# Optimization experiments

Measured on AMD Instinct MI355X. Metric: run time of the kernel, lower is better.

Reference implementation:

```python
import jax, jax.numpy as jnp
import numpy as np

HID = 512
NB = 20
N = 65536
EPS = 1e-5


def layer_norm(x, g, b):
    m = jnp.mean(x, axis=-1, keepdims=True)
    v = jnp.mean(jnp.square(x - m), axis=-1, keepdims=True)
    return (x - m) * jax.lax.rsqrt(v + EPS) * g + b


def setup_inputs() -> dict:
    key = jax.random.key(0)
    ks = jax.random.split(key, 8)
    s = 0.02
    return {
        "x": jax.random.normal(ks[0], (N, 2), dtype=jnp.float32),
        "in_w": jax.random.normal(ks[1], (2, HID), dtype=jnp.float32) * s,
        "in_b": jnp.zeros((HID,), jnp.float32),
        "ln1_g": jnp.ones((NB, HID), jnp.float32),
        "ln1_b": jnp.zeros((NB, HID), jnp.float32),
        "fc1_w": jax.random.normal(ks[2], (NB, HID, HID), dtype=jnp.float32) * s,
        "fc1_b": jnp.zeros((NB, HID), jnp.float32),
        "ln2_g": jnp.ones((NB, HID), jnp.float32),
        "ln2_b": jnp.zeros((NB, HID), jnp.float32),
        "fc2_w": jax.random.normal(ks[3], (NB, HID, HID), dtype=jnp.float32) * s,
        "fc2_b": jnp.zeros((NB, HID), jnp.float32),
        "out_ln_g": jnp.ones((HID,), jnp.float32),
        "out_ln_b": jnp.zeros((HID,), jnp.float32),
        "out_w": jax.random.normal(ks[4], (HID, 1), dtype=jnp.float32) * s,
        "out_b": jnp.zeros((1,), jnp.float32),
    }


def reference(x, in_w, in_b, ln1_g, ln1_b, fc1_w, fc1_b, ln2_g, ln2_b,
              fc2_w, fc2_b, out_ln_g, out_ln_b, out_w, out_b):
    # in_proj + SiLU: [N,2] @ [2,HID]
    h = jax.nn.silu(x @ in_w + in_b)

    def block(h, p):
        g1, b1, w1, c1, g2, b2, w2, c2 = p
        t = jax.nn.silu(layer_norm(h, g1, b1) @ w1 + c1)
        t = layer_norm(t, g2, b2) @ w2 + c2
        return h + t, None

    h, _ = jax.lax.scan(block, h, (ln1_g, ln1_b, fc1_w, fc1_b,
                                   ln2_g, ln2_b, fc2_w, fc2_b))
    h = jax.nn.silu(layer_norm(h, out_ln_g, out_ln_b))
    return h @ out_w + out_b  # [N, 1]
```

## Files before the change

kernel.cpp:

```cpp
#include <hip/hip_runtime.h>


typedef float  fvec4 __attribute__((ext_vector_type(4)));
typedef __bf16 bvec8 __attribute__((ext_vector_type(8)));

#define HN_STRIDE 520
#define PL_STRIDE 67
#define N_PCOL    256
#define WCHUNK    16384
#define SMEM_BYTES (64*HN_STRIDE*2 + N_PCOL*PL_STRIDE*4 + 64*8)

__device__ __forceinline__ unsigned int f2bf(float v) {
    unsigned int u = __float_as_uint(v);
    return (u + 0x7fffu + ((u >> 16) & 1u)) >> 16;
}
__device__ __forceinline__ float silu_f(float v) {
    return v * (1.0f / (1.0f + __expf(-v)));
}

__global__ __launch_bounds__(256) void pack_weights(
        const float* __restrict__ w1, const float* __restrict__ w2,
        unsigned short* __restrict__ pk) {
    int tid = blockIdx.x * 256 + threadIdx.x;
    int l  = tid & 63;
    int f  = tid >> 6;
    int t  = f & 1;
    int kc = (f >> 1) & 15;
    int w  = (f >> 5) & 15;
    int g  = (f >> 9) & 1;
    int b  = f >> 10;
    const float* src = g ? w2 : w1;
    int k0 = kc * 32 + (l >> 4) * 8;
    int n  = w * 32 + (l & 15) * 2 + t;
    const float* s = src + ((size_t)b * 512 + k0) * 512 + n;
    unsigned int r[4];
#pragma unroll
    for (int j = 0; j < 4; ++j) {
        unsigned int lo = f2bf(s[(size_t)(2*j) * 512]);
        unsigned int hi = f2bf(s[(size_t)(2*j + 1) * 512]);
        r[j] = lo | (hi << 16);
    }
    *(uint4*)(pk + (size_t)tid * 8) = make_uint4(r[0], r[1], r[2], r[3]);
}

template <typename GetF>
__device__ __forceinline__ void ln_stats(GetF get, unsigned int* plane,
                                         float2* mv, int pcol, int q, int tid) {
#pragma unroll
    for (int rb = 0; rb < 4; ++rb)
#pragma unroll
        for (int i = 0; i < 4; ++i) {
            float v0 = get(rb, i, 0), v1 = get(rb, i, 1);
            float s  = v0 + v1;
            float ss = v0 * v0 + v1 * v1;
            int row = rb * 16 + q * 4 + i;
            plane[pcol * PL_STRIDE + row] = f2bf(s) | (f2bf(ss) << 16);
        }
    __syncthreads();
    if (tid < 512) {
        int r = tid >> 3, j = tid & 7;
        float s = 0.f, ss = 0.f;
#pragma unroll
        for (int u = 0; u < 32; ++u) {
            unsigned int pv = plane[(j + 8 * u) * PL_STRIDE + r];
            s  += __uint_as_float(pv << 16);
            ss += __uint_as_float(pv & 0xFFFF0000u);
        }
        s += __shfl_xor(s, 1); ss += __shfl_xor(ss, 1);
        s += __shfl_xor(s, 2); ss += __shfl_xor(ss, 2);
        s += __shfl_xor(s, 4); ss += __shfl_xor(ss, 4);
        if (j == 0) {
            float mean = s * (1.f / 512.f);
            float var  = ss * (1.f / 512.f) - mean * mean;
            mv[r] = make_float2(mean, rsqrtf(var + 1e-5f));
        }
    }
    __syncthreads();
}

template <typename GetF>
__device__ __forceinline__ void write_norm(GetF get, unsigned short* hn,
                                           const float2* mv, float2 g, float2 bv,
                                           int colbase, int q) {
#pragma unroll
    for (int rb = 0; rb < 4; ++rb)
#pragma unroll
        for (int i = 0; i < 4; ++i) {
            int row = rb * 16 + q * 4 + i;
            float2 m = mv[row];
            float v0 = (get(rb, i, 0) - m.x) * m.y * g.x + bv.x;
            float v1 = (get(rb, i, 1) - m.x) * m.y * g.y + bv.y;
            *(unsigned int*)(hn + row * HN_STRIDE + colbase) =
                f2bf(v0) | (f2bf(v1) << 16);
        }
    __syncthreads();
}

__device__ __forceinline__ void do_gemm(fvec4 acc[4][2],
                                        const unsigned short* hn,
                                        const unsigned short* __restrict__ wp,
                                        int l, int c, int q) {
#pragma unroll 2
    for (int kc = 0; kc < 16; ++kc) {
        bvec8 a[4], bb[2];
#pragma unroll
        for (int rb = 0; rb < 4; ++rb)
            a[rb] = *(const bvec8*)(hn + (rb * 16 + c) * HN_STRIDE + kc * 32 + q * 8);
#pragma unroll
        for (int t = 0; t < 2; ++t)
            bb[t] = *(const bvec8*)(wp + (kc * 2 + t) * 512 + l * 8);
#pragma unroll
        for (int rb = 0; rb < 4; ++rb)
#pragma unroll
            for (int t = 0; t < 2; ++t)
                acc[rb][t] = __builtin_amdgcn_mfma_f32_16x16x32_bf16(
                    a[rb], bb[t], acc[rb][t], 0, 0, 0);
    }
}

__global__ __launch_bounds__(1024, 4) void mlp_fused(
        const float* __restrict__ x,
        const float* __restrict__ in_w,  const float* __restrict__ in_b,
        const float* __restrict__ ln1_g, const float* __restrict__ ln1_b,
        const float* __restrict__ fc1_b,
        const float* __restrict__ ln2_g, const float* __restrict__ ln2_b,
        const float* __restrict__ fc2_b,
        const float* __restrict__ out_ln_g, const float* __restrict__ out_ln_b,
        const float* __restrict__ out_w, const float* __restrict__ out_b,
        const unsigned short* __restrict__ wpk,
        float* __restrict__ out) {
    extern __shared__ char smem[];
    unsigned short* hn = (unsigned short*)smem;
    unsigned int* plane = (unsigned int*)(smem + 64 * HN_STRIDE * 2);
    float* planef = (float*)plane;
    float2* mv = (float2*)(smem + 64 * HN_STRIDE * 2 + N_PCOL * PL_STRIDE * 4);

    const int tid = threadIdx.x;
    const int w = tid >> 6;
    const int l = tid & 63, c = l & 15, q = l >> 4;
    const int colbase = w * 32 + c * 2;
    const int pcol = w * 16 + c;
    const int row0 = blockIdx.x * 64;

    float h[4][4][2];

    {
        float2 iw0 = *(const float2*)(in_w + colbase);
        float2 iw1 = *(const float2*)(in_w + 512 + colbase);
        float2 ib  = *(const float2*)(in_b + colbase);
#pragma unroll
        for (int rb = 0; rb < 4; ++rb)
#pragma unroll
            for (int i = 0; i < 4; ++i) {
                int row = rb * 16 + q * 4 + i;
                float2 xv = *(const float2*)(x + (size_t)(row0 + row) * 2);
                h[rb][i][0] = silu_f(xv.x * iw0.x + xv.y * iw1.x + ib.x);
                h[rb][i][1] = silu_f(xv.x * iw0.y + xv.y * iw1.y + ib.y);
            }
    }

    auto getH = [&](int rb, int i, int t) { return h[rb][i][t]; };

    for (int b = 0; b < 20; ++b) {
        float2 g1 = *(const float2*)(ln1_g + b * 512 + colbase);
        float2 b1 = *(const float2*)(ln1_b + b * 512 + colbase);
        float2 c1 = *(const float2*)(fc1_b + b * 512 + colbase);
        float2 g2 = *(const float2*)(ln2_g + b * 512 + colbase);
        float2 b2 = *(const float2*)(ln2_b + b * 512 + colbase);
        float2 c2 = *(const float2*)(fc2_b + b * 512 + colbase);
        float c1v[2] = {c1.x, c1.y};
        float c2v[2] = {c2.x, c2.y};

        ln_stats(getH, plane, mv, pcol, q, tid);
        write_norm(getH, hn, mv, g1, b1, colbase, q);

        fvec4 acc[4][2];
#pragma unroll
        for (int rb = 0; rb < 4; ++rb)
#pragma unroll
            for (int t = 0; t < 2; ++t) acc[rb][t] = (fvec4){0.f, 0.f, 0.f, 0.f};
        do_gemm(acc, hn, wpk + ((size_t)(b * 2 + 0) * 16 + w) * WCHUNK, l, c, q);

#pragma unroll
        for (int rb = 0; rb < 4; ++rb)
#pragma unroll
            for (int t = 0; t < 2; ++t)
#pragma unroll
                for (int i = 0; i < 4; ++i)
                    acc[rb][t][i] = silu_f(acc[rb][t][i] + c1v[t]);

        auto getA = [&](int rb, int i, int t) { return acc[rb][t][i]; };
        ln_stats(getA, plane, mv, pcol, q, tid);
        write_norm(getA, hn, mv, g2, b2, colbase, q);

#pragma unroll
        for (int rb = 0; rb < 4; ++rb)
#pragma unroll
            for (int t = 0; t < 2; ++t)
#pragma unroll
                for (int i = 0; i < 4; ++i)
                    acc[rb][t][i] = h[rb][i][t] + c2v[t];
        do_gemm(acc, hn, wpk + ((size_t)(b * 2 + 1) * 16 + w) * WCHUNK, l, c, q);

#pragma unroll
        for (int rb = 0; rb < 4; ++rb)
#pragma unroll
            for (int i = 0; i < 4; ++i)
#pragma unroll
                for (int t = 0; t < 2; ++t)
                    h[rb][i][t] = acc[rb][t][i];
    }

    ln_stats(getH, plane, mv, pcol, q, tid);
    {
        float2 og = *(const float2*)(out_ln_g + colbase);
        float2 ob = *(const float2*)(out_ln_b + colbase);
        float2 ow = *(const float2*)(out_w + colbase);
#pragma unroll
        for (int rb = 0; rb < 4; ++rb)
#pragma unroll
            for (int i = 0; i < 4; ++i) {
                int row = rb * 16 + q * 4 + i;
                float2 m = mv[row];
                float v0 = (h[rb][i][0] - m.x) * m.y * og.x + ob.x;
                float v1 = (h[rb][i][1] - m.x) * m.y * og.y + ob.y;
                float p = silu_f(v0) * ow.x + silu_f(v1) * ow.y;
                planef[pcol * PL_STRIDE + row] = p;
            }
    }
    __syncthreads();
    if (tid < 512) {
        int r = tid >> 3, j = tid & 7;
        float s = 0.f;
#pragma unroll
        for (int u = 0; u < 32; ++u)
            s += planef[(j + 8 * u) * PL_STRIDE + r];
        s += __shfl_xor(s, 1);
        s += __shfl_xor(s, 2);
        s += __shfl_xor(s, 4);
        if (j == 0) out[row0 + r] = s + out_b[0];
    }
}

extern "C" void kernel_launch(void* const* d_in, const int* in_sizes, int n_in,
                              void* d_out, int out_size, void* d_ws, size_t ws_size,
                              hipStream_t stream) {
    const float* x        = (const float*)d_in[0];
    const float* in_w     = (const float*)d_in[1];
    const float* in_b     = (const float*)d_in[2];
    const float* ln1_g    = (const float*)d_in[3];
    const float* ln1_b    = (const float*)d_in[4];
    const float* fc1_w    = (const float*)d_in[5];
    const float* fc1_b    = (const float*)d_in[6];
    const float* ln2_g    = (const float*)d_in[7];
    const float* ln2_b    = (const float*)d_in[8];
    const float* fc2_w    = (const float*)d_in[9];
    const float* fc2_b    = (const float*)d_in[10];
    const float* out_ln_g = (const float*)d_in[11];
    const float* out_ln_b = (const float*)d_in[12];
    const float* out_w    = (const float*)d_in[13];
    const float* out_b    = (const float*)d_in[14];
    float* out = (float*)d_out;
    unsigned short* wpk = (unsigned short*)d_ws;

    (void)hipFuncSetAttribute((const void*)mlp_fused,
                              hipFuncAttributeMaxDynamicSharedMemorySize, SMEM_BYTES);

    pack_weights<<<5120, 256, 0, stream>>>(fc1_w, fc2_w, wpk);
    mlp_fused<<<1024, 1024, SMEM_BYTES, stream>>>(
        x, in_w, in_b, ln1_g, ln1_b, fc1_b, ln2_g, ln2_b, fc2_b,
        out_ln_g, out_ln_b, out_w, out_b, wpk, out);
}
```

Baseline: 2.078 ms.

## Fold LayerNorm affine into weights and apply normalization after GEMM

The LayerNorm gain is folded into the packed bf16 weights, and the beta and bias terms are precomputed as per-column vectors u and v by a new make_uv kernel. The block writes the raw activations to shared memory while it computes row statistics in the same pass, then applies mean and rstd as a per-row affine correction on the GEMM outputs. This removes the separate normalize-and-write pass and one barrier per LayerNorm, and lets the stats reduction use all 1024 threads. The cost is a small extra precompute kernel and a precision risk: unnormalized activations are fed through bf16 and the mean correction involves cancellation.

```diff
diff --git a/kernel.cpp b/kernel.cpp
--- a/kernel.cpp
+++ b/kernel.cpp
@@ -9,6 +9,7 @@
 #define N_PCOL    256
 #define WCHUNK    16384
 #define SMEM_BYTES (64*HN_STRIDE*2 + N_PCOL*PL_STRIDE*4 + 64*8)
+#define WPK_USHORTS ((size_t)20*2*16*WCHUNK)
 
 __device__ __forceinline__ unsigned int f2bf(float v) {
     unsigned int u = __float_as_uint(v);
@@ -20,6 +21,7 @@
 
 __global__ __launch_bounds__(256) void pack_weights(
         const float* __restrict__ w1, const float* __restrict__ w2,
+        const float* __restrict__ g1, const float* __restrict__ g2,
         unsigned short* __restrict__ pk) {
     int tid = blockIdx.x * 256 + threadIdx.x;
     int l  = tid & 63;
@@ -30,70 +32,63 @@
     int g  = (f >> 9) & 1;
     int b  = f >> 10;
     const float* src = g ? w2 : w1;
+    const float* gs  = (g ? g2 : g1) + b * 512;
     int k0 = kc * 32 + (l >> 4) * 8;
     int n  = w * 32 + (l & 15) * 2 + t;
     const float* s = src + ((size_t)b * 512 + k0) * 512 + n;
     unsigned int r[4];
 #pragma unroll
     for (int j = 0; j < 4; ++j) {
-        unsigned int lo = f2bf(s[(size_t)(2*j) * 512]);
-        unsigned int hi = f2bf(s[(size_t)(2*j + 1) * 512]);
+        float ga = gs[k0 + 2 * j];
+        float gb = gs[k0 + 2 * j + 1];
+        unsigned int lo = f2bf(ga * s[(size_t)(2*j) * 512]);
+        unsigned int hi = f2bf(gb * s[(size_t)(2*j + 1) * 512]);
         r[j] = lo | (hi << 16);
     }
     *(uint4*)(pk + (size_t)tid * 8) = make_uint4(r[0], r[1], r[2], r[3]);
 }
 
-template <typename GetF>
-__device__ __forceinline__ void ln_stats(GetF get, unsigned int* plane,
-                                         float2* mv, int pcol, int q, int tid) {
-#pragma unroll
-    for (int rb = 0; rb < 4; ++rb)
-#pragma unroll
-        for (int i = 0; i < 4; ++i) {
-            float v0 = get(rb, i, 0), v1 = get(rb, i, 1);
-            float s  = v0 + v1;
-            float ss = v0 * v0 + v1 * v1;
-            int row = rb * 16 + q * 4 + i;
-            plane[pcol * PL_STRIDE + row] = f2bf(s) | (f2bf(ss) << 16);
-        }
-    __syncthreads();
-    if (tid < 512) {
-        int r = tid >> 3, j = tid & 7;
-        float s = 0.f, ss = 0.f;
-#pragma unroll
-        for (int u = 0; u < 32; ++u) {
-            unsigned int pv = plane[(j + 8 * u) * PL_STRIDE + r];
-            s  += __uint_as_float(pv << 16);
-            ss += __uint_as_float(pv & 0xFFFF0000u);
-        }
-        s += __shfl_xor(s, 1); ss += __shfl_xor(ss, 1);
-        s += __shfl_xor(s, 2); ss += __shfl_xor(ss, 2);
-        s += __shfl_xor(s, 4); ss += __shfl_xor(ss, 4);
-        if (j == 0) {
-            float mean = s * (1.f / 512.f);
-            float var  = ss * (1.f / 512.f) - mean * mean;
-            mv[r] = make_float2(mean, rsqrtf(var + 1e-5f));
-        }
-    }
-    __syncthreads();
-}
-
-template <typename GetF>
-__device__ __forceinline__ void write_norm(GetF get, unsigned short* hn,
-                                           const float2* mv, float2 g, float2 bv,
-                                           int colbase, int q) {
-#pragma unroll
-    for (int rb = 0; rb < 4; ++rb)
-#pragma unroll
-        for (int i = 0; i < 4; ++i) {
-            int row = rb * 16 + q * 4 + i;
-            float2 m = mv[row];
-            float v0 = (get(rb, i, 0) - m.x) * m.y * g.x + bv.x;
-            float v1 = (get(rb, i, 1) - m.x) * m.y * g.y + bv.y;
-            *(unsigned int*)(hn + row * HN_STRIDE + colbase) =
-                f2bf(v0) | (f2bf(v1) << 16);
-        }
-    __syncthreads();
+__global__ __launch_bounds__(512) void make_uv(
+        const float* __restrict__ w1, const float* __restrict__ w2,
+        const float* __restrict__ g1, const float* __restrict__ bl1,
+        const float* __restrict__ cb1,
+        const float* __restrict__ g2, const float* __restrict__ bl2,
+        const float* __restrict__ cb2,
+        float* __restrict__ uv) {
+    int b = blockIdx.x >> 1, slot = blockIdx.x & 1, n = threadIdx.x;
+    const float* W  = (slot ? w2 : w1) + (size_t)b * 512 * 512;
+    const float* g  = (slot ? g2 : g1) + b * 512;
+    const float* bl = (slot ? bl2 : bl1) + b * 512;
+    const float* cb = (slot ? cb2 : cb1) + b * 512;
+    float u = 0.f, v = 0.f;
+    for (int j = 0; j < 512; ++j) {
+        float wv = W[(size_t)j * 512 + n];
+        u = fmaf(g[j], wv, u);
+        v = fmaf(bl[j], wv, v);
+    }
+    uv[((b * 2 + slot) * 2 + 0) * 512 + n] = u;
+    uv[((b * 2 + slot) * 2 + 1) * 512 + n] = v + cb[n];
+}
+
+__device__ __forceinline__ void reduce_mv(const unsigned int* plane,
+                                          float2* mv, int tid) {
+    int r = tid >> 4, j = tid & 15;
+    float s = 0.f, ss = 0.f;
+#pragma unroll
+    for (int u = 0; u < 16; ++u) {
+        unsigned int pv = plane[(j + 16 * u) * PL_STRIDE + r];
+        s  += __uint_as_float(pv << 16);
+        ss += __uint_as_float(pv & 0xFFFF0000u);
+    }
+    s += __shfl_xor(s, 1); ss += __shfl_xor(ss, 1);
+    s += __shfl_xor(s, 2); ss += __shfl_xor(ss, 2);
+    s += __shfl_xor(s, 4); ss += __shfl_xor(ss, 4);
+    s += __shfl_xor(s, 8); ss += __shfl_xor(ss, 8);
+    if (j == 0) {
+        float mean = s * (1.f / 512.f);
+        float var  = ss * (1.f / 512.f) - mean * mean;
+        mv[r] = make_float2(mean, rsqrtf(var + 1e-5f));
+    }
 }
 
 __device__ __forceinline__ void do_gemm(fvec4 acc[4][2],
@@ -121,13 +116,10 @@
 __global__ __launch_bounds__(1024, 4) void mlp_fused(
         const float* __restrict__ x,
         const float* __restrict__ in_w,  const float* __restrict__ in_b,
-        const float* __restrict__ ln1_g, const float* __restrict__ ln1_b,
-        const float* __restrict__ fc1_b,
-        const float* __restrict__ ln2_g, const float* __restrict__ ln2_b,
-        const float* __restrict__ fc2_b,
         const float* __restrict__ out_ln_g, const float* __restrict__ out_ln_b,
         const float* __restrict__ out_w, const float* __restrict__ out_b,
         const unsigned short* __restrict__ wpk,
+        const float* __restrict__ uv,
         float* __restrict__ out) {
     extern __shared__ char smem[];
     unsigned short* hn = (unsigned short*)smem;
@@ -159,20 +151,25 @@
             }
     }
 
-    auto getH = [&](int rb, int i, int t) { return h[rb][i][t]; };
-
     for (int b = 0; b < 20; ++b) {
-        float2 g1 = *(const float2*)(ln1_g + b * 512 + colbase);
-        float2 b1 = *(const float2*)(ln1_b + b * 512 + colbase);
-        float2 c1 = *(const float2*)(fc1_b + b * 512 + colbase);
-        float2 g2 = *(const float2*)(ln2_g + b * 512 + colbase);
-        float2 b2 = *(const float2*)(ln2_b + b * 512 + colbase);
-        float2 c2 = *(const float2*)(fc2_b + b * 512 + colbase);
-        float c1v[2] = {c1.x, c1.y};
-        float c2v[2] = {c2.x, c2.y};
-
-        ln_stats(getH, plane, mv, pcol, q, tid);
-        write_norm(getH, hn, mv, g1, b1, colbase, q);
+        float2 u1  = *(const float2*)(uv + ((b * 2 + 0) * 2 + 0) * 512 + colbase);
+        float2 vc1 = *(const float2*)(uv + ((b * 2 + 0) * 2 + 1) * 512 + colbase);
+        float2 u2  = *(const float2*)(uv + ((b * 2 + 1) * 2 + 0) * 512 + colbase);
+        float2 vc2 = *(const float2*)(uv + ((b * 2 + 1) * 2 + 1) * 512 + colbase);
+
+#pragma unroll
+        for (int rb = 0; rb < 4; ++rb)
+#pragma unroll
+            for (int i = 0; i < 4; ++i) {
+                int row = rb * 16 + q * 4 + i;
+                float v0 = h[rb][i][0], v1 = h[rb][i][1];
+                plane[pcol * PL_STRIDE + row] =
+                    f2bf(v0 + v1) | (f2bf(__builtin_fmaf(v0, v0, v1 * v1)) << 16);
+                *(unsigned int*)(hn + row * HN_STRIDE + colbase) =
+                    f2bf(v0) | (f2bf(v1) << 16);
+            }
+        __syncthreads();
+        reduce_mv(plane, mv, tid);
 
         fvec4 acc[4][2];
 #pragma unroll
@@ -180,38 +177,60 @@
 #pragma unroll
             for (int t = 0; t < 2; ++t) acc[rb][t] = (fvec4){0.f, 0.f, 0.f, 0.f};
         do_gemm(acc, hn, wpk + ((size_t)(b * 2 + 0) * 16 + w) * WCHUNK, l, c, q);
-
-#pragma unroll
-        for (int rb = 0; rb < 4; ++rb)
-#pragma unroll
-            for (int t = 0; t < 2; ++t)
-#pragma unroll
-                for (int i = 0; i < 4; ++i)
-                    acc[rb][t][i] = silu_f(acc[rb][t][i] + c1v[t]);
-
-        auto getA = [&](int rb, int i, int t) { return acc[rb][t][i]; };
-        ln_stats(getA, plane, mv, pcol, q, tid);
-        write_norm(getA, hn, mv, g2, b2, colbase, q);
-
-#pragma unroll
-        for (int rb = 0; rb < 4; ++rb)
-#pragma unroll
-            for (int t = 0; t < 2; ++t)
-#pragma unroll
-                for (int i = 0; i < 4; ++i)
-                    acc[rb][t][i] = h[rb][i][t] + c2v[t];
+        __syncthreads();
+
+#pragma unroll
+        for (int rb = 0; rb < 4; ++rb)
+#pragma unroll
+            for (int i = 0; i < 4; ++i) {
+                int row = rb * 16 + q * 4 + i;
+                float2 m = mv[row];
+                float minv = -m.x * m.y;
+                float t0 = silu_f(__builtin_fmaf(acc[rb][0][i], m.y,
+                                  __builtin_fmaf(minv, u1.x, vc1.x)));
+                float t1 = silu_f(__builtin_fmaf(acc[rb][1][i], m.y,
+                                  __builtin_fmaf(minv, u1.y, vc1.y)));
+                plane[pcol * PL_STRIDE + row] =
+                    f2bf(t0 + t1) | (f2bf(__builtin_fmaf(t0, t0, t1 * t1)) << 16);
+                *(unsigned int*)(hn + row * HN_STRIDE + colbase) =
+                    f2bf(t0) | (f2bf(t1) << 16);
+            }
+        __syncthreads();
+        reduce_mv(plane, mv, tid);
+
+#pragma unroll
+        for (int rb = 0; rb < 4; ++rb)
+#pragma unroll
+            for (int t = 0; t < 2; ++t) acc[rb][t] = (fvec4){0.f, 0.f, 0.f, 0.f};
         do_gemm(acc, hn, wpk + ((size_t)(b * 2 + 1) * 16 + w) * WCHUNK, l, c, q);
-
-#pragma unroll
-        for (int rb = 0; rb < 4; ++rb)
-#pragma unroll
-            for (int i = 0; i < 4; ++i)
-#pragma unroll
-                for (int t = 0; t < 2; ++t)
-                    h[rb][i][t] = acc[rb][t][i];
-    }
-
-    ln_stats(getH, plane, mv, pcol, q, tid);
+        __syncthreads();
+
+#pragma unroll
+        for (int rb = 0; rb < 4; ++rb)
+#pragma unroll
+            for (int i = 0; i < 4; ++i) {
+                int row = rb * 16 + q * 4 + i;
+                float2 m = mv[row];
+                float minv = -m.x * m.y;
+                h[rb][i][0] = __builtin_fmaf(acc[rb][0][i], m.y,
+                    h[rb][i][0] + __builtin_fmaf(minv, u2.x, vc2.x));
+                h[rb][i][1] = __builtin_fmaf(acc[rb][1][i], m.y,
+                    h[rb][i][1] + __builtin_fmaf(minv, u2.y, vc2.y));
+            }
+    }
+
+#pragma unroll
+    for (int rb = 0; rb < 4; ++rb)
+#pragma unroll
+        for (int i = 0; i < 4; ++i) {
+            int row = rb * 16 + q * 4 + i;
+            float v0 = h[rb][i][0], v1 = h[rb][i][1];
+            plane[pcol * PL_STRIDE + row] =
+                f2bf(v0 + v1) | (f2bf(__builtin_fmaf(v0, v0, v1 * v1)) << 16);
+        }
+    __syncthreads();
+    reduce_mv(plane, mv, tid);
+    __syncthreads();
     {
         float2 og = *(const float2*)(out_ln_g + colbase);
         float2 ob = *(const float2*)(out_ln_b + colbase);
@@ -224,20 +243,20 @@
                 float2 m = mv[row];
                 float v0 = (h[rb][i][0] - m.x) * m.y * og.x + ob.x;
                 float v1 = (h[rb][i][1] - m.x) * m.y * og.y + ob.y;
-                float p = silu_f(v0) * ow.x + silu_f(v1) * ow.y;
-                planef[pcol * PL_STRIDE + row] = p;
+                planef[pcol * PL_STRIDE + row] = silu_f(v0) * ow.x + silu_f(v1) * ow.y;
             }
     }
     __syncthreads();
-    if (tid < 512) {
-        int r = tid >> 3, j = tid & 7;
+    {
+        int r = tid >> 4, j = tid & 15;
         float s = 0.f;
 #pragma unroll
-        for (int u = 0; u < 32; ++u)
-            s += planef[(j + 8 * u) * PL_STRIDE + r];
+        for (int u = 0; u < 16; ++u)
+            s += planef[(j + 16 * u) * PL_STRIDE + r];
         s += __shfl_xor(s, 1);
         s += __shfl_xor(s, 2);
         s += __shfl_xor(s, 4);
+        s += __shfl_xor(s, 8);
         if (j == 0) out[row0 + r] = s + out_b[0];
     }
 }
@@ -262,12 +281,14 @@
     const float* out_b    = (const float*)d_in[14];
     float* out = (float*)d_out;
     unsigned short* wpk = (unsigned short*)d_ws;
+    float* uv = (float*)((char*)d_ws + WPK_USHORTS * 2);
 
     (void)hipFuncSetAttribute((const void*)mlp_fused,
                               hipFuncAttributeMaxDynamicSharedMemorySize, SMEM_BYTES);
 
-    pack_weights<<<5120, 256, 0, stream>>>(fc1_w, fc2_w, wpk);
+    pack_weights<<<5120, 256, 0, stream>>>(fc1_w, fc2_w, ln1_g, ln2_g, wpk);
+    make_uv<<<40, 512, 0, stream>>>(fc1_w, fc2_w, ln1_g, ln1_b, fc1_b,
+                                    ln2_g, ln2_b, fc2_b, uv);
     mlp_fused<<<1024, 1024, SMEM_BYTES, stream>>>(
-        x, in_w, in_b, ln1_g, ln1_b, fc1_b, ln2_g, ln2_b, fc2_b,
-        out_ln_g, out_ln_b, out_w, out_b, wpk, out);
-}
+        x, in_w, in_b, out_ln_g, out_ln_b, out_w, out_b, wpk, uv, out);
+}
```

Result: faster. 1.990 ms (-4.3%).
